# Performance work log

Hardware: AMD Instinct MI355X
Metric: run time of the kernel (lower is better)

## Reference

```python
import jax, jax.numpy as jnp
import numpy as np

N = 50000   # nodes
E = 800000  # edges (avg degree 16)
F = 128     # feature dim (input = hidden = output)
H = 8       # heads
D = F // H  # head dim = 16
L = 4       # layers


def setup_inputs() -> dict:
    key = jax.random.key(0)
    ks = jax.random.split(key, 11)
    x = jax.random.normal(ks[0], (N, F), dtype=jnp.float32)
    edge_index = jax.random.randint(ks[1], (2, E), 0, N, dtype=jnp.int64)
    s = 1.0 / np.sqrt(F)
    Wq = jax.random.normal(ks[2], (L, F, F), dtype=jnp.float32) * s
    Wk = jax.random.normal(ks[3], (L, F, F), dtype=jnp.float32) * s
    Wv = jax.random.normal(ks[4], (L, F, F), dtype=jnp.float32) * s
    Ws = jax.random.normal(ks[5], (L, F, F), dtype=jnp.float32) * s  # lin_skip (root weight)
    bq = jax.random.normal(ks[6], (L, F), dtype=jnp.float32) * 0.02
    bk = jax.random.normal(ks[7], (L, F), dtype=jnp.float32) * 0.02
    bv = jax.random.normal(ks[8], (L, F), dtype=jnp.float32) * 0.02
    bs = jax.random.normal(ks[9], (L, F), dtype=jnp.float32) * 0.02
    return {"x": x, "edge_index": edge_index, "Wq": Wq, "bq": bq,
            "Wk": Wk, "bk": bk, "Wv": Wv, "bv": bv, "Ws": Ws, "bs": bs}


def _transformer_conv(x, src, dst, Wq, bq, Wk, bk, Wv, bv, Ws, bs):
    # Q from destination nodes, K/V from source nodes (PyG TransformerConv).
    q = (x @ Wq + bq)[dst].reshape(E, H, D)
    k = (x @ Wk + bk)[src].reshape(E, H, D)
    alpha = (q * k).sum(-1) * (1.0 / np.sqrt(D))            # [E, H]
    # segment softmax over edges grouped by destination node
    amax = jax.ops.segment_max(alpha, dst, num_segments=N)   # [N, H]
    amax = jnp.where(jnp.isfinite(amax), amax, 0.0)
    p = jnp.exp(alpha - amax[dst])
    denom = jax.ops.segment_sum(p, dst, num_segments=N)      # [N, H]
    a = p / denom[dst]                                       # [E, H]
    v = (x @ Wv + bv)[src].reshape(E, H, D)
    msg = (a[..., None] * v).reshape(E, F)
    out = jax.ops.segment_sum(msg, dst, num_segments=N)      # concat heads
    out = out + x @ Ws + bs                                  # root/skip connection
    return out, a


def reference(x, edge_index, Wq, bq, Wk, bk, Wv, bv, Ws, bs):
    src, dst = edge_index[0], edge_index[1]
    alphas = []
    h = x
    for i in range(L - 1):
        h, a = _transformer_conv(h, src, dst, Wq[i], bq[i], Wk[i], bk[i],
                                 Wv[i], bv[i], Ws[i], bs[i])
        h = jax.nn.gelu(h, approximate=False)
        alphas.append(a)
    h, a = _transformer_conv(h, src, dst, Wq[-1], bq[-1], Wk[-1], bk[-1],
                             Wv[-1], bv[-1], Ws[-1], bs[-1])
    alphas.append(a)
    return h, jnp.stack(alphas)  # [N, F], [L, E, H]
```

## Files before the change

kernel.cpp:

```cpp
#include <hip/hip_runtime.h>
#include <math.h>

#define F 128
#define HEADS 8

typedef __attribute__((ext_vector_type(8))) short short8;
typedef __attribute__((ext_vector_type(4))) float floatx4;

__device__ __forceinline__ unsigned short f2bf(float f) {
    unsigned u = __float_as_uint(f);
    unsigned r = u + 0x7FFFu + ((u >> 16) & 1u);
    return (unsigned short)(r >> 16);
}
__device__ __forceinline__ float bf2f(unsigned short u) {
    return __uint_as_float(((unsigned)u) << 16);
}
__device__ __forceinline__ float bflo(unsigned u) { return __uint_as_float(u << 16); }
__device__ __forceinline__ float bfhi(unsigned u) { return __uint_as_float(u & 0xffff0000u); }


__global__ __launch_bounds__(256) void hist_k(const int* __restrict__ dst, int E, int* __restrict__ deg) {
    int e = blockIdx.x * 256 + threadIdx.x;
    if (e < E) atomicAdd(&deg[dst[e]], 1);
}

__global__ __launch_bounds__(256) void scan1_k(const int* __restrict__ deg, int N,
                                               int* __restrict__ start, int* __restrict__ partials) {
    __shared__ int sm[256];
    int t = threadIdx.x;
    int i = blockIdx.x * 256 + t;
    int v = (i < N) ? deg[i] : 0;
    sm[t] = v;
    __syncthreads();
    for (int off = 1; off < 256; off <<= 1) {
        int add = (t >= off) ? sm[t - off] : 0;
        __syncthreads();
        sm[t] += add;
        __syncthreads();
    }
    if (i < N) start[i] = sm[t] - v;
    if (t == 255) partials[blockIdx.x] = sm[t];
}

__global__ __launch_bounds__(256) void scan2_k(int* __restrict__ partials, int nb,
                                               int* __restrict__ start, int N, int E) {
    __shared__ int sm[256];
    int t = threadIdx.x;
    int v = (t < nb) ? partials[t] : 0;
    sm[t] = v;
    __syncthreads();
    for (int off = 1; off < 256; off <<= 1) {
        int add = (t >= off) ? sm[t - off] : 0;
        __syncthreads();
        sm[t] += add;
        __syncthreads();
    }
    if (t < nb) partials[t] = sm[t] - v;
    if (t == 0) start[N] = E;
}

__global__ __launch_bounds__(256) void scan3_k(int* __restrict__ start, int N, const int* __restrict__ partials) {
    int i = blockIdx.x * 256 + threadIdx.x;
    if (i < N) start[i] += partials[blockIdx.x];
}

__global__ __launch_bounds__(256) void fill_k(const int* __restrict__ src, const int* __restrict__ dst, int E,
                                              const int* __restrict__ start, int* __restrict__ cursor,
                                              int2* __restrict__ epair) {
    int e = blockIdx.x * 256 + threadIdx.x;
    if (e < E) {
        int dd = dst[e];
        int pos = atomicAdd(&cursor[dd], 1);
        epair[start[dd] + pos] = make_int2(e, src[e]);
    }
}

__global__ __launch_bounds__(256) void cvt_k(const float* __restrict__ x, unsigned short* __restrict__ xb, int total4) {
    int i = blockIdx.x * 256 + threadIdx.x;
    if (i < total4) {
        float4 v = ((const float4*)x)[i];
        ushort4 o;
        o.x = f2bf(v.x); o.y = f2bf(v.y); o.z = f2bf(v.z); o.w = f2bf(v.w);
        ((ushort4*)xb)[i] = o;
    }
}


__global__ __launch_bounds__(256) void wprep_k(
    const float* __restrict__ Wq, const float* __restrict__ Wk,
    const float* __restrict__ Wv, const float* __restrict__ Ws,
    unsigned short* __restrict__ out, int total) {
    int idx = blockIdx.x * 256 + threadIdx.x;
    if (idx >= total) return;
    int j = idx & 7;
    int lane = (idx >> 3) & 63;
    int rest = idx >> 9;
    int chunk = rest & 3;
    int ftile = (rest >> 2) & 7;
    int mat = (rest >> 5) & 3;
    int layer = rest >> 7;
    int k = chunk * 32 + (lane >> 4) * 8 + j;
    int f = ftile * 16 + (lane & 15);
    const float* W = (mat == 0) ? Wq : (mat == 1) ? Wk : (mat == 2) ? Wv : Ws;
    out[idx] = f2bf(W[((size_t)layer * F + k) * F + f]);
}


__global__ __launch_bounds__(256) void gemm_mfma(
    const unsigned short* __restrict__ xb, const unsigned short* __restrict__ wfrag,
    const float* __restrict__ bq, const float* __restrict__ bk,
    const float* __restrict__ bv, const float* __restrict__ bs,
    float* __restrict__ Q, unsigned short* __restrict__ Kb,
    unsigned short* __restrict__ Vb, float* __restrict__ S, int N) {
    int wave = threadIdx.x >> 6;
    int lane = threadIdx.x & 63;
    int row0 = blockIdx.x * 32;
    int lm = lane & 15, quad = lane >> 4;
    const unsigned short* wf = wfrag + wave * 16384;

    floatx4 acc[2][8];
#pragma unroll
    for (int t = 0; t < 2; t++)
#pragma unroll
        for (int u = 0; u < 8; u++) acc[t][u] = (floatx4){0.f, 0.f, 0.f, 0.f};

#pragma unroll
    for (int chunk = 0; chunk < 4; chunk++) {
        short8 xfr[2];
#pragma unroll
        for (int t = 0; t < 2; t++) {
            int m = row0 + t * 16 + lm;
            m = (m < N) ? m : (N - 1);
            xfr[t] = *(const short8*)(xb + (size_t)m * F + chunk * 32 + quad * 8);
        }
#pragma unroll
        for (int u = 0; u < 8; u++) {
            short8 wfr = *(const short8*)(wf + ((u * 4 + chunk) * 64 + lane) * 8);
            acc[0][u] = __builtin_amdgcn_mfma_f32_16x16x32_bf16(wfr, xfr[0], acc[0][u], 0, 0, 0);
            acc[1][u] = __builtin_amdgcn_mfma_f32_16x16x32_bf16(wfr, xfr[1], acc[1][u], 0, 0, 0);
        }
    }

    const float* bias = (wave == 0) ? bq : (wave == 1) ? bk : (wave == 2) ? bv : bs;
#pragma unroll
    for (int u = 0; u < 8; u++) {
        float4 bv4 = *(const float4*)&bias[u * 16 + quad * 4];
#pragma unroll
        for (int t = 0; t < 2; t++) {
            int node = row0 + t * 16 + lm;
            if (node < N) {
                floatx4 a = acc[t][u];
                size_t off = (size_t)node * F + u * 16 + quad * 4;
                float v0 = a[0] + bv4.x, v1 = a[1] + bv4.y, v2 = a[2] + bv4.z, v3 = a[3] + bv4.w;
                if (wave == 0) {
                    *(float4*)&Q[off] = make_float4(v0, v1, v2, v3);
                } else if (wave == 1) {
                    ushort4 o = {f2bf(v0), f2bf(v1), f2bf(v2), f2bf(v3)};
                    *(ushort4*)&Kb[off] = o;
                } else if (wave == 2) {
                    ushort4 o = {f2bf(v0), f2bf(v1), f2bf(v2), f2bf(v3)};
                    *(ushort4*)&Vb[off] = o;
                } else {
                    *(float4*)&S[off] = make_float4(v0, v1, v2, v3);
                }
            }
        }
    }
}


__device__ __forceinline__ float gelu_exact(float v) {
    return 0.5f * v * (1.0f + erff(v * 0.70710678118654752f));
}

__global__ __launch_bounds__(256) void edge_k(
    const float* __restrict__ Q, const unsigned short* __restrict__ Kb,
    const unsigned short* __restrict__ Vb, const float* __restrict__ S,
    const int* __restrict__ start, const int2* __restrict__ epair,
    float* __restrict__ aout, float* __restrict__ md,
    float* __restrict__ hout_f, unsigned short* __restrict__ hout_b,
    int N, int do_gelu) {
    __shared__ float wbuf[4][64][8];
    __shared__ int sbuf[4][64];
    __shared__ float mdbuf[4][8];

    int wv = threadIdx.x >> 6;
    int lane = threadIdx.x & 63;
    int n = blockIdx.x * 4 + wv;
    if (n >= N) return;

    int beg = start[n], end = start[n + 1];
    int slot = lane >> 3, h = lane & 7;
    int g = lane >> 4, fl = lane & 15;
    int fh = fl >> 1;

    const float* qp = Q + (size_t)n * F + h * 16;
    float4 q0 = *(const float4*)(qp + 0);
    float4 q1 = *(const float4*)(qp + 4);
    float4 q2 = *(const float4*)(qp + 8);
    float4 q3 = *(const float4*)(qp + 12);

    float d = 0.f;
    float a0 = 0.f, a1 = 0.f, a2 = 0.f, a3 = 0.f, a4 = 0.f, a5 = 0.f, a6 = 0.f, a7 = 0.f;

    for (int c0 = beg; c0 < end; c0 += 64) {
        int cnt = min(64, end - c0);

        int nit = (cnt + 7) >> 3;
        for (int it = 0; it < nit; it++) {
            int idx = it * 8 + slot;
            bool val = idx < cnt;
            int gi = c0 + (val ? idx : 0);
            int2 pe = epair[gi];
            int s = pe.y;
            const unsigned short* kp = Kb + (size_t)s * F + h * 16;
            uint4 ka = *(const uint4*)(kp);
            uint4 kc = *(const uint4*)(kp + 8);
            float p = q0.x * bflo(ka.x) + q0.y * bfhi(ka.x)
                    + q0.z * bflo(ka.y) + q0.w * bfhi(ka.y)
                    + q1.x * bflo(ka.z) + q1.y * bfhi(ka.z)
                    + q1.z * bflo(ka.w) + q1.w * bfhi(ka.w)
                    + q2.x * bflo(kc.x) + q2.y * bfhi(kc.x)
                    + q2.z * bflo(kc.y) + q2.w * bfhi(kc.y)
                    + q3.x * bflo(kc.z) + q3.y * bfhi(kc.z)
                    + q3.z * bflo(kc.w) + q3.w * bfhi(kc.w);
            float w = __expf(p * 0.25f);
            if (!val) w = 0.f;
            d += w;
            wbuf[wv][idx][h] = w;
            if (h == 0) sbuf[wv][idx] = s;
            if (val) aout[(size_t)pe.x * HEADS + h] = w;
        }

        for (int j = 0; j < cnt; j += 8) {
            int idx0 = j + g;
            int idx1 = j + 4 + g;
            bool v0 = idx0 < cnt;
            bool v1 = idx1 < cnt;
            int s0 = sbuf[wv][v0 ? idx0 : 0];
            int s1 = sbuf[wv][v1 ? idx1 : 0];
            float w0 = wbuf[wv][v0 ? idx0 : 0][fh];
            float w1 = wbuf[wv][v1 ? idx1 : 0][fh];
            if (!v0) w0 = 0.f;
            if (!v1) w1 = 0.f;
            uint4 va = *(const uint4*)&Vb[(size_t)s0 * F + fl * 8];
            uint4 vb2 = *(const uint4*)&Vb[(size_t)s1 * F + fl * 8];
            a0 += w0 * bflo(va.x); a1 += w0 * bfhi(va.x);
            a2 += w0 * bflo(va.y); a3 += w0 * bfhi(va.y);
            a4 += w0 * bflo(va.z); a5 += w0 * bfhi(va.z);
            a6 += w0 * bflo(va.w); a7 += w0 * bfhi(va.w);
            a0 += w1 * bflo(vb2.x); a1 += w1 * bfhi(vb2.x);
            a2 += w1 * bflo(vb2.y); a3 += w1 * bfhi(vb2.y);
            a4 += w1 * bflo(vb2.z); a5 += w1 * bfhi(vb2.z);
            a6 += w1 * bflo(vb2.w); a7 += w1 * bfhi(vb2.w);
        }
    }

    d += __shfl_xor(d, 8);
    d += __shfl_xor(d, 16);
    d += __shfl_xor(d, 32);
    float inv_d = (d > 0.f) ? 1.f / d : 0.f;
    if (slot == 0) {
        md[(size_t)n * HEADS + h] = inv_d;
        mdbuf[wv][h] = inv_d;
    }

    a0 += __shfl_xor(a0, 16); a0 += __shfl_xor(a0, 32);
    a1 += __shfl_xor(a1, 16); a1 += __shfl_xor(a1, 32);
    a2 += __shfl_xor(a2, 16); a2 += __shfl_xor(a2, 32);
    a3 += __shfl_xor(a3, 16); a3 += __shfl_xor(a3, 32);
    a4 += __shfl_xor(a4, 16); a4 += __shfl_xor(a4, 32);
    a5 += __shfl_xor(a5, 16); a5 += __shfl_xor(a5, 32);
    a6 += __shfl_xor(a6, 16); a6 += __shfl_xor(a6, 32);
    a7 += __shfl_xor(a7, 16); a7 += __shfl_xor(a7, 32);

    if (lane < 16) {
        float invd = mdbuf[wv][fh];
        const float* sp = S + (size_t)n * F + fl * 8;
        float4 s0 = *(const float4*)(sp + 0);
        float4 s1 = *(const float4*)(sp + 4);
        float o0 = a0 * invd + s0.x, o1 = a1 * invd + s0.y;
        float o2 = a2 * invd + s0.z, o3 = a3 * invd + s0.w;
        float o4 = a4 * invd + s1.x, o5 = a5 * invd + s1.y;
        float o6 = a6 * invd + s1.z, o7 = a7 * invd + s1.w;
        if (do_gelu) {
            o0 = gelu_exact(o0); o1 = gelu_exact(o1); o2 = gelu_exact(o2); o3 = gelu_exact(o3);
            o4 = gelu_exact(o4); o5 = gelu_exact(o5); o6 = gelu_exact(o6); o7 = gelu_exact(o7);
            uint4 ob;
            ob.x = (unsigned)f2bf(o0) | ((unsigned)f2bf(o1) << 16);
            ob.y = (unsigned)f2bf(o2) | ((unsigned)f2bf(o3) << 16);
            ob.z = (unsigned)f2bf(o4) | ((unsigned)f2bf(o5) << 16);
            ob.w = (unsigned)f2bf(o6) | ((unsigned)f2bf(o7) << 16);
            *(uint4*)&hout_b[(size_t)n * F + fl * 8] = ob;
        } else {
            float* op = hout_f + (size_t)n * F + fl * 8;
            *(float4*)(op + 0) = make_float4(o0, o1, o2, o3);
            *(float4*)(op + 4) = make_float4(o4, o5, o6, o7);
        }
    }
}


__global__ __launch_bounds__(256) void norm_k(float* __restrict__ a, const float* __restrict__ md,
                                              const int* __restrict__ dst, int E8) {
    int i = blockIdx.x * 256 + threadIdx.x;
    if (i < E8) {
        int e = i >> 3;
        int h = i & 7;
        a[i] *= md[(size_t)dst[e] * HEADS + h];
    }
}


extern "C" void kernel_launch(void* const* d_in, const int* in_sizes, int n_in,
                              void* d_out, int out_size, void* d_ws, size_t ws_size,
                              hipStream_t stream) {
    const float* x  = (const float*)d_in[0];
    const int*   ei = (const int*)d_in[1];
    const float* Wq = (const float*)d_in[2];
    const float* bq = (const float*)d_in[3];
    const float* Wk = (const float*)d_in[4];
    const float* bk = (const float*)d_in[5];
    const float* Wv = (const float*)d_in[6];
    const float* bv = (const float*)d_in[7];
    const float* Ws = (const float*)d_in[8];
    const float* bs = (const float*)d_in[9];

    const int N = in_sizes[0] / F;
    const int E = in_sizes[1] / 2;
    const int L = in_sizes[2] / (F * F);

    float* Qb = (float*)d_ws;
    float* Sb = Qb + (size_t)N * F;
    float* md = Sb + (size_t)N * F;
    unsigned short* xb = (unsigned short*)(md + (size_t)N * HEADS);
    unsigned short* hb = xb + (size_t)N * F;
    unsigned short* Kb = hb + (size_t)N * F;
    unsigned short* Vb = Kb + (size_t)N * F;
    unsigned short* wfrag = Vb + (size_t)N * F;
    int* start = (int*)(wfrag + (size_t)L * 4 * 16384);
    int* cursor = start + (N + 1);
    int2* epair = (int2*)(cursor + N);
    int* partials = (int*)(epair + E);

    float* out_h = (float*)d_out;
    float* out_a = out_h + (size_t)N * F;

    const int* srcIdx = ei;
    const int* dstIdx = ei + E;

    int nbScan = (N + 255) / 256;
    hipMemsetAsync(cursor, 0, sizeof(int) * N, stream);
    hist_k<<<(E + 255) / 256, 256, 0, stream>>>(dstIdx, E, cursor);
    scan1_k<<<nbScan, 256, 0, stream>>>(cursor, N, start, partials);
    scan2_k<<<1, 256, 0, stream>>>(partials, nbScan, start, N, E);
    scan3_k<<<nbScan, 256, 0, stream>>>(start, N, partials);
    hipMemsetAsync(cursor, 0, sizeof(int) * N, stream);
    fill_k<<<(E + 255) / 256, 256, 0, stream>>>(srcIdx, dstIdx, E, start, cursor, epair);

    int wtotal = L * 4 * 16384;
    wprep_k<<<(wtotal + 255) / 256, 256, 0, stream>>>(Wq, Wk, Wv, Ws, wfrag, wtotal);
    cvt_k<<<((N * F / 4) + 255) / 256, 256, 0, stream>>>(x, xb, N * F / 4);

    for (int l = 0; l < L; ++l) {
        const unsigned short* hin = (l == 0) ? xb : hb;
        gemm_mfma<<<(N + 31) / 32, 256, 0, stream>>>(
            hin, wfrag + (size_t)l * 4 * 16384,
            bq + (size_t)l * F, bk + (size_t)l * F,
            bv + (size_t)l * F, bs + (size_t)l * F,
            Qb, Kb, Vb, Sb, N);
        edge_k<<<(N + 3) / 4, 256, 0, stream>>>(
            Qb, Kb, Vb, Sb, start, epair,
            out_a + (size_t)l * E * HEADS, md, out_h, hb, N, (l < L - 1) ? 1 : 0);
        norm_k<<<((E * HEADS) + 255) / 256, 256, 0, stream>>>(
            out_a + (size_t)l * E * HEADS, md, dstIdx, E * HEADS);
    }
}
```

Baseline: 806.5 us.

## Fuse attention normalization into edge kernel and store Q/K/V as fp16 with fdot2

Removes the separate norm_k pass by buffering edge ids and weights in shared memory and writing already-normalized attention coefficients directly when degree fits in one 64-edge chunk, with a read-modify-write fallback otherwise. Q, K and V are now written as packed fp16 instead of fp32/bf16, and the Q·K dot product uses fdot2 instructions. This cuts a full pass over the E×H alpha array per layer and halves Q traffic, at the cost of fp16 range/precision risk on projections.

```diff
diff --git a/kernel.cpp b/kernel.cpp
--- a/kernel.cpp
+++ b/kernel.cpp
@@ -6,17 +6,26 @@
 
 typedef __attribute__((ext_vector_type(8))) short short8;
 typedef __attribute__((ext_vector_type(4))) float floatx4;
+typedef __attribute__((ext_vector_type(2))) _Float16 half2v;
 
 __device__ __forceinline__ unsigned short f2bf(float f) {
     unsigned u = __float_as_uint(f);
     unsigned r = u + 0x7FFFu + ((u >> 16) & 1u);
     return (unsigned short)(r >> 16);
 }
-__device__ __forceinline__ float bf2f(unsigned short u) {
-    return __uint_as_float(((unsigned)u) << 16);
-}
-__device__ __forceinline__ float bflo(unsigned u) { return __uint_as_float(u << 16); }
-__device__ __forceinline__ float bfhi(unsigned u) { return __uint_as_float(u & 0xffff0000u); }
+
+__device__ __forceinline__ half2v ashalf2(unsigned u) {
+    return __builtin_bit_cast(half2v, u);
+}
+__device__ __forceinline__ unsigned pkh(float a, float b) {
+    return __builtin_bit_cast(unsigned, __builtin_amdgcn_cvt_pkrtz(a, b));
+}
+
+#if __has_builtin(__builtin_amdgcn_fdot2)
+#define FDOT2(a, b, c) __builtin_amdgcn_fdot2((a), (b), (c), false)
+#else
+#define FDOT2(a, b, c) ((c) + (float)(a)[0] * (float)(b)[0] + (float)(a)[1] * (float)(b)[1])
+#endif
 
 
 __global__ __launch_bounds__(256) void hist_k(const int* __restrict__ dst, int E, int* __restrict__ deg) {
@@ -110,8 +119,8 @@
     const unsigned short* __restrict__ xb, const unsigned short* __restrict__ wfrag,
     const float* __restrict__ bq, const float* __restrict__ bk,
     const float* __restrict__ bv, const float* __restrict__ bs,
-    float* __restrict__ Q, unsigned short* __restrict__ Kb,
-    unsigned short* __restrict__ Vb, float* __restrict__ S, int N) {
+    unsigned short* __restrict__ Qh, unsigned short* __restrict__ Kh,
+    unsigned short* __restrict__ Vh, float* __restrict__ S, int N) {
     int wave = threadIdx.x >> 6;
     int lane = threadIdx.x & 63;
     int row0 = blockIdx.x * 32;
@@ -152,16 +161,11 @@
                 floatx4 a = acc[t][u];
                 size_t off = (size_t)node * F + u * 16 + quad * 4;
                 float v0 = a[0] + bv4.x, v1 = a[1] + bv4.y, v2 = a[2] + bv4.z, v3 = a[3] + bv4.w;
-                if (wave == 0) {
-                    *(float4*)&Q[off] = make_float4(v0, v1, v2, v3);
-                } else if (wave == 1) {
-                    ushort4 o = {f2bf(v0), f2bf(v1), f2bf(v2), f2bf(v3)};
-                    *(ushort4*)&Kb[off] = o;
-                } else if (wave == 2) {
-                    ushort4 o = {f2bf(v0), f2bf(v1), f2bf(v2), f2bf(v3)};
-                    *(ushort4*)&Vb[off] = o;
+                if (wave == 3) {
+                    *(float4*)&S[off] = make_float4(v0, v1, v2, v3);
                 } else {
-                    *(float4*)&S[off] = make_float4(v0, v1, v2, v3);
+                    unsigned short* dp = (wave == 0) ? Qh : (wave == 1) ? Kh : Vh;
+                    *(uint2*)&dp[off] = make_uint2(pkh(v0, v1), pkh(v2, v3));
                 }
             }
         }
@@ -174,14 +178,15 @@
 }
 
 __global__ __launch_bounds__(256) void edge_k(
-    const float* __restrict__ Q, const unsigned short* __restrict__ Kb,
-    const unsigned short* __restrict__ Vb, const float* __restrict__ S,
+    const unsigned short* __restrict__ Qh, const unsigned short* __restrict__ Kh,
+    const unsigned short* __restrict__ Vh, const float* __restrict__ S,
     const int* __restrict__ start, const int2* __restrict__ epair,
-    float* __restrict__ aout, float* __restrict__ md,
+    float* __restrict__ aout,
     float* __restrict__ hout_f, unsigned short* __restrict__ hout_b,
     int N, int do_gelu) {
     __shared__ float wbuf[4][64][8];
     __shared__ int sbuf[4][64];
+    __shared__ int ebuf[4][64];
     __shared__ float mdbuf[4][8];
 
     int wv = threadIdx.x >> 6;
@@ -190,15 +195,17 @@
     if (n >= N) return;
 
     int beg = start[n], end = start[n + 1];
+    int deg = end - beg;
+    bool multi = deg > 64;
     int slot = lane >> 3, h = lane & 7;
     int g = lane >> 4, fl = lane & 15;
     int fh = fl >> 1;
 
-    const float* qp = Q + (size_t)n * F + h * 16;
-    float4 q0 = *(const float4*)(qp + 0);
-    float4 q1 = *(const float4*)(qp + 4);
-    float4 q2 = *(const float4*)(qp + 8);
-    float4 q3 = *(const float4*)(qp + 12);
+    const unsigned short* qp = Qh + (size_t)n * F + h * 16;
+    uint4 qa = *(const uint4*)(qp);
+    uint4 qc = *(const uint4*)(qp + 8);
+    half2v q0 = ashalf2(qa.x), q1 = ashalf2(qa.y), q2 = ashalf2(qa.z), q3 = ashalf2(qa.w);
+    half2v q4 = ashalf2(qc.x), q5 = ashalf2(qc.y), q6 = ashalf2(qc.z), q7 = ashalf2(qc.w);
 
     float d = 0.f;
     float a0 = 0.f, a1 = 0.f, a2 = 0.f, a3 = 0.f, a4 = 0.f, a5 = 0.f, a6 = 0.f, a7 = 0.f;
@@ -213,23 +220,24 @@
             int gi = c0 + (val ? idx : 0);
             int2 pe = epair[gi];
             int s = pe.y;
-            const unsigned short* kp = Kb + (size_t)s * F + h * 16;
+            const unsigned short* kp = Kh + (size_t)s * F + h * 16;
             uint4 ka = *(const uint4*)(kp);
             uint4 kc = *(const uint4*)(kp + 8);
-            float p = q0.x * bflo(ka.x) + q0.y * bfhi(ka.x)
-                    + q0.z * bflo(ka.y) + q0.w * bfhi(ka.y)
-                    + q1.x * bflo(ka.z) + q1.y * bfhi(ka.z)
-                    + q1.z * bflo(ka.w) + q1.w * bfhi(ka.w)
-                    + q2.x * bflo(kc.x) + q2.y * bfhi(kc.x)
-                    + q2.z * bflo(kc.y) + q2.w * bfhi(kc.y)
-                    + q3.x * bflo(kc.z) + q3.y * bfhi(kc.z)
-                    + q3.z * bflo(kc.w) + q3.w * bfhi(kc.w);
-            float w = __expf(p * 0.25f);
+            float p0 = 0.f, p1 = 0.f;
+            p0 = FDOT2(q0, ashalf2(ka.x), p0);
+            p0 = FDOT2(q1, ashalf2(ka.y), p0);
+            p0 = FDOT2(q2, ashalf2(ka.z), p0);
+            p0 = FDOT2(q3, ashalf2(ka.w), p0);
+            p1 = FDOT2(q4, ashalf2(kc.x), p1);
+            p1 = FDOT2(q5, ashalf2(kc.y), p1);
+            p1 = FDOT2(q6, ashalf2(kc.z), p1);
+            p1 = FDOT2(q7, ashalf2(kc.w), p1);
+            float w = __expf((p0 + p1) * 0.25f);
             if (!val) w = 0.f;
             d += w;
             wbuf[wv][idx][h] = w;
-            if (h == 0) sbuf[wv][idx] = s;
-            if (val) aout[(size_t)pe.x * HEADS + h] = w;
+            if (h == 0) { sbuf[wv][idx] = s; ebuf[wv][idx] = pe.x; }
+            if (multi && val) aout[(size_t)pe.x * HEADS + h] = w;
         }
 
         for (int j = 0; j < cnt; j += 8) {
@@ -243,16 +251,18 @@
             float w1 = wbuf[wv][v1 ? idx1 : 0][fh];
             if (!v0) w0 = 0.f;
             if (!v1) w1 = 0.f;
-            uint4 va = *(const uint4*)&Vb[(size_t)s0 * F + fl * 8];
-            uint4 vb2 = *(const uint4*)&Vb[(size_t)s1 * F + fl * 8];
-            a0 += w0 * bflo(va.x); a1 += w0 * bfhi(va.x);
-            a2 += w0 * bflo(va.y); a3 += w0 * bfhi(va.y);
-            a4 += w0 * bflo(va.z); a5 += w0 * bfhi(va.z);
-            a6 += w0 * bflo(va.w); a7 += w0 * bfhi(va.w);
-            a0 += w1 * bflo(vb2.x); a1 += w1 * bfhi(vb2.x);
-            a2 += w1 * bflo(vb2.y); a3 += w1 * bfhi(vb2.y);
-            a4 += w1 * bflo(vb2.z); a5 += w1 * bfhi(vb2.z);
-            a6 += w1 * bflo(vb2.w); a7 += w1 * bfhi(vb2.w);
+            uint4 va = *(const uint4*)&Vh[(size_t)s0 * F + fl * 8];
+            uint4 vb2 = *(const uint4*)&Vh[(size_t)s1 * F + fl * 8];
+            half2v x0 = ashalf2(va.x), x1 = ashalf2(va.y), x2 = ashalf2(va.z), x3 = ashalf2(va.w);
+            half2v y0 = ashalf2(vb2.x), y1 = ashalf2(vb2.y), y2 = ashalf2(vb2.z), y3 = ashalf2(vb2.w);
+            a0 += w0 * (float)x0[0]; a1 += w0 * (float)x0[1];
+            a2 += w0 * (float)x1[0]; a3 += w0 * (float)x1[1];
+            a4 += w0 * (float)x2[0]; a5 += w0 * (float)x2[1];
+            a6 += w0 * (float)x3[0]; a7 += w0 * (float)x3[1];
+            a0 += w1 * (float)y0[0]; a1 += w1 * (float)y0[1];
+            a2 += w1 * (float)y1[0]; a3 += w1 * (float)y1[1];
+            a4 += w1 * (float)y2[0]; a5 += w1 * (float)y2[1];
+            a6 += w1 * (float)y3[0]; a7 += w1 * (float)y3[1];
         }
     }
 
@@ -260,9 +270,14 @@
     d += __shfl_xor(d, 16);
     d += __shfl_xor(d, 32);
     float inv_d = (d > 0.f) ? 1.f / d : 0.f;
-    if (slot == 0) {
-        md[(size_t)n * HEADS + h] = inv_d;
-        mdbuf[wv][h] = inv_d;
+    if (slot == 0) mdbuf[wv][h] = inv_d;
+
+    if (!multi) {
+        for (int idx = slot; idx < deg; idx += 8)
+            aout[(size_t)ebuf[wv][idx] * HEADS + h] = wbuf[wv][idx][h] * inv_d;
+    } else {
+        for (int idx = slot; idx < deg; idx += 8)
+            aout[(size_t)epair[beg + idx].x * HEADS + h] *= inv_d;
     }
 
     a0 += __shfl_xor(a0, 16); a0 += __shfl_xor(a0, 32);
@@ -301,17 +316,6 @@
 }
 
 
-__global__ __launch_bounds__(256) void norm_k(float* __restrict__ a, const float* __restrict__ md,
-                                              const int* __restrict__ dst, int E8) {
-    int i = blockIdx.x * 256 + threadIdx.x;
-    if (i < E8) {
-        int e = i >> 3;
-        int h = i & 7;
-        a[i] *= md[(size_t)dst[e] * HEADS + h];
-    }
-}
-
-
 extern "C" void kernel_launch(void* const* d_in, const int* in_sizes, int n_in,
                               void* d_out, int out_size, void* d_ws, size_t ws_size,
                               hipStream_t stream) {
@@ -330,18 +334,17 @@
     const int E = in_sizes[1] / 2;
     const int L = in_sizes[2] / (F * F);
 
-    float* Qb = (float*)d_ws;
-    float* Sb = Qb + (size_t)N * F;
-    float* md = Sb + (size_t)N * F;
-    unsigned short* xb = (unsigned short*)(md + (size_t)N * HEADS);
+    float* Sb = (float*)d_ws;
+    unsigned short* Qh = (unsigned short*)(Sb + (size_t)N * F);
+    unsigned short* xb = Qh + (size_t)N * F;
     unsigned short* hb = xb + (size_t)N * F;
     unsigned short* Kb = hb + (size_t)N * F;
     unsigned short* Vb = Kb + (size_t)N * F;
     unsigned short* wfrag = Vb + (size_t)N * F;
-    int* start = (int*)(wfrag + (size_t)L * 4 * 16384);
+    int2* epair = (int2*)(wfrag + (size_t)L * 4 * 16384);
+    int* start = (int*)(epair + E);
     int* cursor = start + (N + 1);
-    int2* epair = (int2*)(cursor + N);
-    int* partials = (int*)(epair + E);
+    int* partials = cursor + N;
 
     float* out_h = (float*)d_out;
     float* out_a = out_h + (size_t)N * F;
@@ -368,11 +371,9 @@
             hin, wfrag + (size_t)l * 4 * 16384,
             bq + (size_t)l * F, bk + (size_t)l * F,
             bv + (size_t)l * F, bs + (size_t)l * F,
-            Qb, Kb, Vb, Sb, N);
+            Qh, Kb, Vb, Sb, N);
         edge_k<<<(N + 3) / 4, 256, 0, stream>>>(
-            Qb, Kb, Vb, Sb, start, epair,
-            out_a + (size_t)l * E * HEADS, md, out_h, hb, N, (l < L - 1) ? 1 : 0);
-        norm_k<<<((E * HEADS) + 255) / 256, 256, 0, stream>>>(
-            out_a + (size_t)l * E * HEADS, md, dstIdx, E * HEADS);
-    }
-}
+            Qh, Kb, Vb, Sb, start, epair,
+            out_a + (size_t)l * E * HEADS, out_h, hb, N, (l < L - 1) ? 1 : 0);
+    }
+}
```

After: 685.8 us. -15.0%, faster.
